# Kernel tuning notes

Hardware: AMD Instinct MI355X
Metric: run time of the kernel (lower is better)

## Reference

```python
import jax, jax.numpy as jnp
import numpy as np

B, T = 65536, 200
H, S, P = 512, 1000, 5
EPS = 1e-6


def setup_inputs() -> dict:
    key = jax.random.key(0)
    ks = jax.random.split(key, 8)
    init = lambda k, shp, fan: (jax.random.normal(k, shp, jnp.float32) / np.float32(np.sqrt(fan)))
    return {
        "X": jax.random.randint(ks[0], (B,), 0, S, dtype=jnp.int32),
        "y": jax.random.randint(ks[1], (B, T), 0, 2, dtype=jnp.int32),
        "embed": init(ks[2], (S, H), 1.0),
        "W1": init(ks[3], (H, H), H), "b1": jnp.zeros((H,), jnp.float32),
        "W2": init(ks[4], (H, H), H), "b2": jnp.zeros((H,), jnp.float32),
        "Wout": init(ks[5], (H, P), H), "bout": jnp.zeros((P,), jnp.float32),
    }


def reference(X, y, embed, W1, b1, W2, b2, Wout, bout):
    # --- MLP over skill embeddings: params (B, 5) = (l, f, g, s, latent0) ---
    e = embed[X]                                    # (B, H)
    h = jax.nn.relu(e @ W1 + b1)                    # num_layers = 2
    h = jax.nn.relu(h @ W2 + b2)
    params = jnp.clip(jax.nn.sigmoid(h @ Wout + bout), EPS, 1.0 - EPS)  # (B, 5)
    l, g, s = params[:, 0], params[:, 2], params[:, 3]
    latent0 = params[:, 4]                          # (B,)

    y_clean = jnp.where(y == -1, 0, y).astype(jnp.float32)  # (B, T)

    # --- BKT latent-update recurrence over T steps ---
    def step(latent, y_t):
        num1 = latent * (1.0 - s)
        correct = num1 + (1.0 - latent) * g
        k_t1 = num1 / correct
        k_t0 = latent * s / (latent * s + (1.0 - latent) * (1.0 - g))
        k_t = jnp.where(y_t > 0.5, k_t1, k_t0)
        nxt = jnp.clip(k_t + (1.0 - k_t) * l, EPS, 1.0 - EPS)
        return nxt, (correct, latent)

    _, (corrects, latents) = jax.lax.scan(step, latent0, y_clean.T)  # (T, B) each
    return corrects.T, latents.T, params
```

## Files before the change

### kernel.cpp

```cpp
#include <hip/hip_runtime.h>


typedef unsigned int uint;
typedef unsigned short ushort_t;
typedef __attribute__((ext_vector_type(8))) short short8;
typedef __attribute__((ext_vector_type(4))) float f32x4;

#define SS 1000
#define HH 512
#define TT 200
#define BB_ 65536
#define PP 5

#define OFF_EMB   0
#define OFF_B1    512000
#define OFF_B2    512512
#define OFF_WOUT  513024
#define OFF_BOUT  515584
#define CONV_TOT  515589

__device__ __forceinline__ float b2f(ushort_t u) {
    return __uint_as_float(((uint)u) << 16);
}
__device__ __forceinline__ ushort_t f2b(float f) {
    uint u = __float_as_uint(f);
    uint r = u + 0x7FFFu + ((u >> 16) & 1u);
    return (ushort_t)(r >> 16);
}
__device__ __forceinline__ int detect_bf16(const uint* __restrict__ embed_raw,
                                           int tid) {
    uint w = embed_raw[tid & 63];
    uint e = (w >> 7) & 0xFFu;
    bool pl = (e >= 117u && e <= 130u);
    return __popcll(__ballot(pl)) >= 32 ? 1 : 0;
}
__device__ __forceinline__ ushort_t ld_bf16(const void* src, int idx, int fb) {
    return fb ? ((const ushort_t*)src)[idx] : f2b(((const float*)src)[idx]);
}

__device__ __forceinline__ float bkt_step(float latent, bool yt,
                                          float oms, float omg, float A1,
                                          float A0, float g, float s,
                                          float oml, float l,
                                          float* correct_out) {
    float num1    = latent * oms;
    float correct = fmaf(latent, A1, g);
    float lats    = latent * s;
    float num = yt ? num1 : lats;
    float den = yt ? correct : fmaf(latent, A0, omg);
    float kt  = num * __builtin_amdgcn_rcpf(den);
    *correct_out = correct;
    float nxt = fmaf(kt, oml, l);
    return fminf(fmaxf(nxt, 1e-6f), 1.f - 1e-6f);
}

__global__ __launch_bounds__(256) void prep_kernel(
    const void* __restrict__ embed, const void* __restrict__ W1,
    const void* __restrict__ b1,    const void* __restrict__ W2,
    const void* __restrict__ b2,    const void* __restrict__ Wout,
    const void* __restrict__ bout,
    ushort_t* __restrict__ conv, ushort_t* __restrict__ WT1,
    ushort_t* __restrict__ WT2)
{
    int tid = threadIdx.x;
    int fb = detect_bf16((const uint*)embed, tid);
    int bx = blockIdx.x;
    if (bx < 2015) {
        int i = bx * 256 + tid;
        if (i < CONV_TOT) {
            const void* src; int off;
            if      (i < OFF_B1)   { src = embed; off = i; }
            else if (i < OFF_B2)   { src = b1;    off = i - OFF_B1; }
            else if (i < OFF_WOUT) { src = b2;    off = i - OFF_B2; }
            else if (i < OFF_BOUT) { src = Wout;  off = i - OFF_WOUT; }
            else                   { src = bout;  off = i - OFF_BOUT; }
            conv[i] = ld_bf16(src, off, fb);
        }
    } else {
        __shared__ ushort_t t[32][33];
        int bi = bx - 2015;
        const void* W = bi < 256 ? W1 : W2;
        ushort_t* WT = bi < 256 ? WT1 : WT2;
        int ti = bi & 255;
        int k0 = (ti & 15) * 32, n0 = (ti >> 4) * 32;
        int tx = tid & 31, ty = tid >> 5;
        #pragma unroll
        for (int i = ty; i < 32; i += 8)
            t[i][tx] = ld_bf16(W, (k0 + i) * HH + n0 + tx, fb);
        __syncthreads();
        #pragma unroll
        for (int i = ty; i < 32; i += 8)
            WT[(n0 + i) * HH + k0 + tx] = t[tx][i];
    }
}

__global__ __launch_bounds__(256) void mlp_layer(
    const ushort_t* __restrict__ A, const ushort_t* __restrict__ WT,
    const ushort_t* __restrict__ bias, ushort_t* __restrict__ H, int Mclamp)
{
    int tid = threadIdx.x;
    int lane = tid & 63;
    int wave = tid >> 6;
    int m_base = blockIdx.x * 64 + wave * 16;
    int n_base = blockIdx.y * 16;
    int lrow = lane & 15;
    int q = lane >> 4;
    int rowA = m_base + lrow; if (rowA > Mclamp) rowA = Mclamp;

    const short8* Ap = (const short8*)(A + (size_t)rowA * HH) + q;
    const short8* Bp = (const short8*)(WT + (size_t)(n_base + lrow) * HH) + q;

    f32x4 acc = {0.f, 0.f, 0.f, 0.f};
    #pragma unroll 8
    for (int kk = 0; kk < 16; kk++) {
        short8 a = Ap[kk * 4];
        short8 b = Bp[kk * 4];
        acc = __builtin_amdgcn_mfma_f32_16x16x32_bf16(a, b, acc, 0, 0, 0);
    }

    int orow = m_base + q * 4;
    int n = n_base + lrow;
    float bb = b2f(bias[n]);
    #pragma unroll
    for (int r = 0; r < 4; r++) {
        float v = acc[r] + bb;
        H[(size_t)(orow + r) * HH + n] = f2b(fmaxf(v, 0.f));
    }
}

__global__ __launch_bounds__(256) void params_kernel(
    const ushort_t* __restrict__ h2, const ushort_t* __restrict__ conv,
    float* __restrict__ table)
{
    int wid = blockIdx.x * 4 + (threadIdx.x >> 6);
    int lane = threadIdx.x & 63;
    if (wid >= SS * PP) return;
    int row = wid / PP, p = wid - row * PP;
    const ushort_t* Wout = conv + OFF_WOUT;
    const ushort_t* bout = conv + OFF_BOUT;
    const short8* hr = (const short8*)(h2 + (size_t)row * HH);
    short8 h = hr[lane];
    float acc = 0.f;
    #pragma unroll
    for (int j = 0; j < 8; j++) {
        int k = lane * 8 + j;
        acc += b2f((ushort_t)h[j]) * b2f(Wout[k * PP + p]);
    }
    #pragma unroll
    for (int m = 32; m; m >>= 1) acc += __shfl_xor(acc, m);
    if (lane == 0) {
        float x = acc + b2f(bout[p]);
        float sg = 1.f / (1.f + expf(-x));
        sg = fminf(fmaxf(sg, 1e-6f), 1.f - 1e-6f);
        table[(size_t)row * 8 + p] = sg;
    }
}

__global__ __launch_bounds__(256) void scan_a(
    const int* __restrict__ X, const int* __restrict__ y,
    const float* __restrict__ table,
    float* __restrict__ cpA, uint* __restrict__ maskA)
{
    int r = blockIdx.x * 256 + threadIdx.x;
    const int4* yrow = (const int4*)(y + (size_t)r * TT);
    uint u[8] = {0, 0, 0, 0, 0, 0, 0, 0};
    #pragma unroll
    for (int k = 0; k < 50; k++) {
        int4 v = yrow[k];
        int t = 4 * k;
        u[(t + 0) / 25] |= (uint)(v.x == 1) << ((t + 0) % 25);
        u[(t + 1) / 25] |= (uint)(v.y == 1) << ((t + 1) % 25);
        u[(t + 2) / 25] |= (uint)(v.z == 1) << ((t + 2) % 25);
        u[(t + 3) / 25] |= (uint)(v.w == 1) << ((t + 3) % 25);
    }

    int xi = X[r]; xi = xi < 0 ? 0 : (xi >= SS ? SS - 1 : xi);
    float l      = table[xi * 8 + 0];
    float g      = table[xi * 8 + 2];
    float s      = table[xi * 8 + 3];
    float latent = table[xi * 8 + 4];
    float oms = 1.f - s, omg = 1.f - g, oml = 1.f - l;
    float A1 = 1.f - s - g, A0 = s + g - 1.f;

    float cp[8];
    #pragma unroll
    for (int w = 0; w < 8; w++) {
        cp[w] = latent;
        uint uw = u[w];
        #pragma unroll
        for (int i = 0; i < 25; i++) {
            float cdummy;
            latent = bkt_step(latent, (uw >> i) & 1u,
                              oms, omg, A1, A0, g, s, oml, l, &cdummy);
        }
    }
    #pragma unroll
    for (int w = 0; w < 8; w++) {
        cpA[(size_t)w * BB_ + r]   = cp[w];
        maskA[(size_t)w * BB_ + r] = u[w];
    }
}

__global__ __launch_bounds__(256) void scan_b(
    const int* __restrict__ X, const float* __restrict__ table,
    const float* __restrict__ cpA, const uint* __restrict__ maskA,
    const uint* __restrict__ embed_raw, void* __restrict__ out)
{
    __shared__ __align__(16) float stg[32 * 200];
    int tid = blockIdx.x * 256 + threadIdx.x;
    int r = tid >> 3;
    int j = tid & 7;
    int lr = threadIdx.x >> 3;
    int rbase = blockIdx.x * 32;
    int fb = detect_bf16(embed_raw, threadIdx.x);

    int xi = X[r]; xi = xi < 0 ? 0 : (xi >= SS ? SS - 1 : xi);
    float l  = table[xi * 8 + 0];
    float p1 = table[xi * 8 + 1];
    float g  = table[xi * 8 + 2];
    float s  = table[xi * 8 + 3];
    float L0 = table[xi * 8 + 4];

    if (j < 5) {
        float pv = j == 0 ? l : j == 1 ? p1 : j == 2 ? g : j == 3 ? s : L0;
        size_t po = 2ull * BB_ * TT + (size_t)r * 5 + j;
        if (fb) ((ushort_t*)out)[po] = f2b(pv);
        else    ((float*)out)[po] = pv;
    }

    float latent = cpA[(size_t)j * BB_ + r];
    uint  u      = maskA[(size_t)j * BB_ + r];
    float oms = 1.f - s, omg = 1.f - g, oml = 1.f - l;
    float A1 = 1.f - s - g, A0 = s + g - 1.f;

    if (fb) {
        ushort_t* cgb = (ushort_t*)out;
        ushort_t* lgb = (ushort_t*)out + (size_t)BB_ * TT;
        size_t eoff = (size_t)r * TT + j * 25;
        #pragma unroll
        for (int i = 0; i < 25; i++) {
            float correct;
            float nxt = bkt_step(latent, (u >> i) & 1u,
                                 oms, omg, A1, A0, g, s, oml, l, &correct);
            cgb[eoff + i] = f2b(correct);
            lgb[eoff + i] = f2b(latent);
            latent = nxt;
        }
        return;
    }

    float lat_arr[25];
    int sbase = lr * 200 + j * 25;
    #pragma unroll
    for (int i = 0; i < 25; i++) {
        float correct;
        float nxt = bkt_step(latent, (u >> i) & 1u,
                             oms, omg, A1, A0, g, s, oml, l, &correct);
        stg[sbase + i] = correct;
        lat_arr[i] = latent;
        latent = nxt;
    }
    __syncthreads();
    {
        const uint4* src = (const uint4*)stg;
        uint4* dst = (uint4*)((float*)out + (size_t)rbase * TT);
        for (int idx = threadIdx.x; idx < 1600; idx += 256)
            dst[idx] = src[idx];
    }
    __syncthreads();
    #pragma unroll
    for (int i = 0; i < 25; i++)
        stg[sbase + i] = lat_arr[i];
    __syncthreads();
    {
        const uint4* src = (const uint4*)stg;
        uint4* dst = (uint4*)((float*)out + (size_t)BB_ * TT + (size_t)rbase * TT);
        for (int idx = threadIdx.x; idx < 1600; idx += 256)
            dst[idx] = src[idx];
    }
}

extern "C" void kernel_launch(void* const* d_in, const int* in_sizes, int n_in,
                              void* d_out, int out_size, void* d_ws, size_t ws_size,
                              hipStream_t stream) {
    const int* X = (const int*)d_in[0];
    const int* y = (const int*)d_in[1];

    char* ws = (char*)d_ws;
    ushort_t* conv  = (ushort_t*)(ws);
    ushort_t* WT1   = (ushort_t*)(ws + 1048576);
    ushort_t* WT2   = (ushort_t*)(ws + 1572864);
    ushort_t* h1    = (ushort_t*)(ws + 2097152);
    ushort_t* h2    = (ushort_t*)(ws + 3145728);
    float*    table = (float*)(ws + 4194304);
    float*    cpA   = (float*)(ws + 4227072);
    uint*     maskA = (uint*)(ws + 6324224);

    prep_kernel<<<dim3(2527, 1, 1), 256, 0, stream>>>(
        d_in[2], d_in[3], d_in[4], d_in[5], d_in[6], d_in[7], d_in[8],
        conv, WT1, WT2);
    mlp_layer<<<dim3(16, 32, 1), 256, 0, stream>>>(conv + OFF_EMB, WT1, conv + OFF_B1, h1, SS - 1);
    mlp_layer<<<dim3(16, 32, 1), 256, 0, stream>>>(h1, WT2, conv + OFF_B2, h2, 1023);
    params_kernel<<<dim3(1250, 1, 1), 256, 0, stream>>>(h2, conv, table);
    scan_a<<<dim3(BB_ / 256, 1, 1), 256, 0, stream>>>(X, y, table, cpA, maskA);
    scan_b<<<dim3((BB_ * 8) / 256, 1, 1), 256, 0, stream>>>(
        X, table, cpA, maskA, (const uint*)d_in[2], (void*)d_out);
}
```

Measured before the change: 208.9 us.

## Fuse MLP prep stages into cooperative kernel and merge scan passes

Prep, both MLP layers and the params projection now run in one cooperative kernel separated by grid syncs, replacing four launches. The two scan kernels become one: each block packs its y rows into shared-memory bits, one thread per row computes the segment checkpoints into shared memory, and 8 threads per row then produce the outputs. This drops the global cpA/maskA round trip and the launch gaps between stages. Output copies use nontemporal stores. The risk is that the checkpoint pass runs serially on 32 threads per block while the other threads wait, which limits parallelism inside each block.

```diff
diff --git a/kernel.cpp b/kernel.cpp
--- a/kernel.cpp
+++ b/kernel.cpp
@@ -1,10 +1,14 @@
 #include <hip/hip_runtime.h>
+#include <hip/hip_cooperative_groups.h>
+namespace cg = cooperative_groups;
 
 
 typedef unsigned int uint;
+typedef unsigned char uchar;
 typedef unsigned short ushort_t;
 typedef __attribute__((ext_vector_type(8))) short short8;
 typedef __attribute__((ext_vector_type(4))) float f32x4;
+typedef __attribute__((ext_vector_type(4))) uint uint4v;
 
 #define SS 1000
 #define HH 512
@@ -54,55 +58,13 @@
     return fminf(fmaxf(nxt, 1e-6f), 1.f - 1e-6f);
 }
 
-__global__ __launch_bounds__(256) void prep_kernel(
-    const void* __restrict__ embed, const void* __restrict__ W1,
-    const void* __restrict__ b1,    const void* __restrict__ W2,
-    const void* __restrict__ b2,    const void* __restrict__ Wout,
-    const void* __restrict__ bout,
-    ushort_t* __restrict__ conv, ushort_t* __restrict__ WT1,
-    ushort_t* __restrict__ WT2)
+__device__ __forceinline__ void mlp_tile(
+    const ushort_t* __restrict__ A, const ushort_t* __restrict__ WT,
+    const ushort_t* __restrict__ bias, ushort_t* __restrict__ H,
+    int Mclamp, int id, int lane)
 {
-    int tid = threadIdx.x;
-    int fb = detect_bf16((const uint*)embed, tid);
-    int bx = blockIdx.x;
-    if (bx < 2015) {
-        int i = bx * 256 + tid;
-        if (i < CONV_TOT) {
-            const void* src; int off;
-            if      (i < OFF_B1)   { src = embed; off = i; }
-            else if (i < OFF_B2)   { src = b1;    off = i - OFF_B1; }
-            else if (i < OFF_WOUT) { src = b2;    off = i - OFF_B2; }
-            else if (i < OFF_BOUT) { src = Wout;  off = i - OFF_WOUT; }
-            else                   { src = bout;  off = i - OFF_BOUT; }
-            conv[i] = ld_bf16(src, off, fb);
-        }
-    } else {
-        __shared__ ushort_t t[32][33];
-        int bi = bx - 2015;
-        const void* W = bi < 256 ? W1 : W2;
-        ushort_t* WT = bi < 256 ? WT1 : WT2;
-        int ti = bi & 255;
-        int k0 = (ti & 15) * 32, n0 = (ti >> 4) * 32;
-        int tx = tid & 31, ty = tid >> 5;
-        #pragma unroll
-        for (int i = ty; i < 32; i += 8)
-            t[i][tx] = ld_bf16(W, (k0 + i) * HH + n0 + tx, fb);
-        __syncthreads();
-        #pragma unroll
-        for (int i = ty; i < 32; i += 8)
-            WT[(n0 + i) * HH + k0 + tx] = t[tx][i];
-    }
-}
-
-__global__ __launch_bounds__(256) void mlp_layer(
-    const ushort_t* __restrict__ A, const ushort_t* __restrict__ WT,
-    const ushort_t* __restrict__ bias, ushort_t* __restrict__ H, int Mclamp)
-{
-    int tid = threadIdx.x;
-    int lane = tid & 63;
-    int wave = tid >> 6;
-    int m_base = blockIdx.x * 64 + wave * 16;
-    int n_base = blockIdx.y * 16;
+    int m_base = (id & 63) * 16;
+    int n_base = (id >> 6) * 16;
     int lrow = lane & 15;
     int q = lane >> 4;
     int rowA = m_base + lrow; if (rowA > Mclamp) rowA = Mclamp;
@@ -117,7 +79,6 @@
         short8 b = Bp[kk * 4];
         acc = __builtin_amdgcn_mfma_f32_16x16x32_bf16(a, b, acc, 0, 0, 0);
     }
-
     int orow = m_base + q * 4;
     int n = n_base + lrow;
     float bb = b2f(bias[n]);
@@ -128,93 +89,126 @@
     }
 }
 
-__global__ __launch_bounds__(256) void params_kernel(
-    const ushort_t* __restrict__ h2, const ushort_t* __restrict__ conv,
-    float* __restrict__ table)
+__global__ __launch_bounds__(256, 2) void aux_kernel(
+    const void* embed, const void* W1, const void* b1, const void* W2,
+    const void* b2, const void* Wout, const void* bout,
+    ushort_t* conv, ushort_t* WT1, ushort_t* WT2,
+    ushort_t* h1, ushort_t* h2, float* table)
 {
-    int wid = blockIdx.x * 4 + (threadIdx.x >> 6);
-    int lane = threadIdx.x & 63;
-    if (wid >= SS * PP) return;
-    int row = wid / PP, p = wid - row * PP;
-    const ushort_t* Wout = conv + OFF_WOUT;
-    const ushort_t* bout = conv + OFF_BOUT;
-    const short8* hr = (const short8*)(h2 + (size_t)row * HH);
-    short8 h = hr[lane];
-    float acc = 0.f;
-    #pragma unroll
-    for (int j = 0; j < 8; j++) {
-        int k = lane * 8 + j;
-        acc += b2f((ushort_t)h[j]) * b2f(Wout[k * PP + p]);
-    }
-    #pragma unroll
-    for (int m = 32; m; m >>= 1) acc += __shfl_xor(acc, m);
-    if (lane == 0) {
-        float x = acc + b2f(bout[p]);
-        float sg = 1.f / (1.f + expf(-x));
-        sg = fminf(fmaxf(sg, 1e-6f), 1.f - 1e-6f);
-        table[(size_t)row * 8 + p] = sg;
-    }
-}
-
-__global__ __launch_bounds__(256) void scan_a(
+    cg::grid_group grid = cg::this_grid();
+    __shared__ ushort_t t[32][33];
+    int tid = threadIdx.x;
+    int bx = blockIdx.x;
+    int lane = tid & 63;
+    int wave = tid >> 6;
+    int fb = detect_bf16((const uint*)embed, tid);
+
+    for (int i = bx * 256 + tid; i < CONV_TOT; i += 512 * 256) {
+        const void* src; int off;
+        if      (i < OFF_B1)   { src = embed; off = i; }
+        else if (i < OFF_B2)   { src = b1;    off = i - OFF_B1; }
+        else if (i < OFF_WOUT) { src = b2;    off = i - OFF_B2; }
+        else if (i < OFF_BOUT) { src = Wout;  off = i - OFF_WOUT; }
+        else                   { src = bout;  off = i - OFF_BOUT; }
+        conv[i] = ld_bf16(src, off, fb);
+    }
+    {
+        const void* W = bx < 256 ? W1 : W2;
+        ushort_t* WT = bx < 256 ? WT1 : WT2;
+        int ti = bx & 255;
+        int k0 = (ti & 15) * 32, n0 = (ti >> 4) * 32;
+        int tx = tid & 31, ty = tid >> 5;
+        #pragma unroll
+        for (int i = ty; i < 32; i += 8)
+            t[i][tx] = ld_bf16(W, (k0 + i) * HH + n0 + tx, fb);
+        __syncthreads();
+        #pragma unroll
+        for (int i = ty; i < 32; i += 8)
+            WT[(n0 + i) * HH + k0 + tx] = t[tx][i];
+    }
+    grid.sync();
+
+    int id = bx * 4 + wave;
+    mlp_tile(conv + OFF_EMB, WT1, conv + OFF_B1, h1, SS - 1, id, lane);
+    grid.sync();
+    mlp_tile(h1, WT2, conv + OFF_B2, h2, 1023, id, lane);
+    grid.sync();
+
+    const ushort_t* WoutC = conv + OFF_WOUT;
+    const ushort_t* boutC = conv + OFF_BOUT;
+    for (int wid = id; wid < SS * PP; wid += 2048) {
+        int row = wid / PP, p = wid - row * PP;
+        const short8* hr = (const short8*)(h2 + (size_t)row * HH);
+        short8 h = hr[lane];
+        float acc = 0.f;
+        #pragma unroll
+        for (int j = 0; j < 8; j++) {
+            int k = lane * 8 + j;
+            acc += b2f((ushort_t)h[j]) * b2f(WoutC[k * PP + p]);
+        }
+        #pragma unroll
+        for (int m = 32; m; m >>= 1) acc += __shfl_xor(acc, m);
+        if (lane == 0) {
+            float x = acc + b2f(boutC[p]);
+            float sg = 1.f / (1.f + expf(-x));
+            sg = fminf(fmaxf(sg, 1e-6f), 1.f - 1e-6f);
+            table[(size_t)row * 8 + p] = sg;
+        }
+    }
+}
+
+__global__ __launch_bounds__(256) void scan_kernel(
     const int* __restrict__ X, const int* __restrict__ y,
-    const float* __restrict__ table,
-    float* __restrict__ cpA, uint* __restrict__ maskA)
-{
-    int r = blockIdx.x * 256 + threadIdx.x;
-    const int4* yrow = (const int4*)(y + (size_t)r * TT);
-    uint u[8] = {0, 0, 0, 0, 0, 0, 0, 0};
-    #pragma unroll
-    for (int k = 0; k < 50; k++) {
-        int4 v = yrow[k];
-        int t = 4 * k;
-        u[(t + 0) / 25] |= (uint)(v.x == 1) << ((t + 0) % 25);
-        u[(t + 1) / 25] |= (uint)(v.y == 1) << ((t + 1) % 25);
-        u[(t + 2) / 25] |= (uint)(v.z == 1) << ((t + 2) % 25);
-        u[(t + 3) / 25] |= (uint)(v.w == 1) << ((t + 3) % 25);
-    }
-
-    int xi = X[r]; xi = xi < 0 ? 0 : (xi >= SS ? SS - 1 : xi);
-    float l      = table[xi * 8 + 0];
-    float g      = table[xi * 8 + 2];
-    float s      = table[xi * 8 + 3];
-    float latent = table[xi * 8 + 4];
-    float oms = 1.f - s, omg = 1.f - g, oml = 1.f - l;
-    float A1 = 1.f - s - g, A0 = s + g - 1.f;
-
-    float cp[8];
-    #pragma unroll
-    for (int w = 0; w < 8; w++) {
-        cp[w] = latent;
-        uint uw = u[w];
-        #pragma unroll
-        for (int i = 0; i < 25; i++) {
-            float cdummy;
-            latent = bkt_step(latent, (uw >> i) & 1u,
-                              oms, omg, A1, A0, g, s, oml, l, &cdummy);
-        }
-    }
-    #pragma unroll
-    for (int w = 0; w < 8; w++) {
-        cpA[(size_t)w * BB_ + r]   = cp[w];
-        maskA[(size_t)w * BB_ + r] = u[w];
-    }
-}
-
-__global__ __launch_bounds__(256) void scan_b(
-    const int* __restrict__ X, const float* __restrict__ table,
-    const float* __restrict__ cpA, const uint* __restrict__ maskA,
-    const uint* __restrict__ embed_raw, void* __restrict__ out)
+    const float* __restrict__ table, const uint* __restrict__ embed_raw,
+    void* __restrict__ out)
 {
     __shared__ __align__(16) float stg[32 * 200];
-    int tid = blockIdx.x * 256 + threadIdx.x;
-    int r = tid >> 3;
-    int j = tid & 7;
-    int lr = threadIdx.x >> 3;
+    __shared__ uchar ybit[32 * 50];
+    __shared__ float cpL[8 * 32];
+    __shared__ uint  maskL[8 * 32];
+    int tid = threadIdx.x;
     int rbase = blockIdx.x * 32;
-    int fb = detect_bf16(embed_raw, threadIdx.x);
-
-    int xi = X[r]; xi = xi < 0 ? 0 : (xi >= SS ? SS - 1 : xi);
+    int fb = detect_bf16(embed_raw, tid);
+
+    for (int idx = tid; idx < 1600; idx += 256) {
+        int r = idx / 50, k = idx - r * 50;
+        int4 v = *(const int4*)(y + (size_t)(rbase + r) * TT + k * 4);
+        uint nib = (uint)(v.x == 1) | ((uint)(v.y == 1) << 1) |
+                   ((uint)(v.z == 1) << 2) | ((uint)(v.w == 1) << 3);
+        ybit[r * 50 + k] = (uchar)nib;
+    }
+    __syncthreads();
+
+    if (tid < 32) {
+        int rg = rbase + tid;
+        int xi = X[rg]; xi = xi < 0 ? 0 : (xi >= SS ? SS - 1 : xi);
+        float l      = table[xi * 8 + 0];
+        float g      = table[xi * 8 + 2];
+        float s      = table[xi * 8 + 3];
+        float latent = table[xi * 8 + 4];
+        float oms = 1.f - s, omg = 1.f - g, oml = 1.f - l;
+        float A1 = 1.f - s - g, A0 = s + g - 1.f;
+        int base = tid * 50;
+        #pragma unroll
+        for (int w = 0; w < 8; w++) {
+            cpL[w * 32 + tid] = latent;
+            uint m = 0;
+            #pragma unroll
+            for (int i = 0; i < 25; i++) {
+                int t_ = w * 25 + i;
+                uint bit = (ybit[base + (t_ >> 2)] >> (t_ & 3)) & 1u;
+                m |= bit << i;
+                float cd;
+                latent = bkt_step(latent, bit, oms, omg, A1, A0, g, s, oml, l, &cd);
+            }
+            maskL[w * 32 + tid] = m;
+        }
+    }
+    __syncthreads();
+
+    int r = tid >> 3, j = tid & 7;
+    int rg = rbase + r;
+    int xi = X[rg]; xi = xi < 0 ? 0 : (xi >= SS ? SS - 1 : xi);
     float l  = table[xi * 8 + 0];
     float p1 = table[xi * 8 + 1];
     float g  = table[xi * 8 + 2];
@@ -223,20 +217,20 @@
 
     if (j < 5) {
         float pv = j == 0 ? l : j == 1 ? p1 : j == 2 ? g : j == 3 ? s : L0;
-        size_t po = 2ull * BB_ * TT + (size_t)r * 5 + j;
+        size_t po = 2ull * BB_ * TT + (size_t)rg * 5 + j;
         if (fb) ((ushort_t*)out)[po] = f2b(pv);
         else    ((float*)out)[po] = pv;
     }
 
-    float latent = cpA[(size_t)j * BB_ + r];
-    uint  u      = maskA[(size_t)j * BB_ + r];
+    float latent = cpL[j * 32 + r];
+    uint  u      = maskL[j * 32 + r];
     float oms = 1.f - s, omg = 1.f - g, oml = 1.f - l;
     float A1 = 1.f - s - g, A0 = s + g - 1.f;
 
     if (fb) {
         ushort_t* cgb = (ushort_t*)out;
         ushort_t* lgb = (ushort_t*)out + (size_t)BB_ * TT;
-        size_t eoff = (size_t)r * TT + j * 25;
+        size_t eoff = (size_t)rg * TT + j * 25;
         #pragma unroll
         for (int i = 0; i < 25; i++) {
             float correct;
@@ -250,7 +244,7 @@
     }
 
     float lat_arr[25];
-    int sbase = lr * 200 + j * 25;
+    int sbase = r * 200 + j * 25;
     #pragma unroll
     for (int i = 0; i < 25; i++) {
         float correct;
@@ -262,10 +256,10 @@
     }
     __syncthreads();
     {
-        const uint4* src = (const uint4*)stg;
-        uint4* dst = (uint4*)((float*)out + (size_t)rbase * TT);
-        for (int idx = threadIdx.x; idx < 1600; idx += 256)
-            dst[idx] = src[idx];
+        const uint4v* src = (const uint4v*)stg;
+        uint4v* dst = (uint4v*)((float*)out + (size_t)rbase * TT);
+        for (int idx = tid; idx < 1600; idx += 256)
+            __builtin_nontemporal_store(src[idx], dst + idx);
     }
     __syncthreads();
     #pragma unroll
@@ -273,10 +267,10 @@
         stg[sbase + i] = lat_arr[i];
     __syncthreads();
     {
-        const uint4* src = (const uint4*)stg;
-        uint4* dst = (uint4*)((float*)out + (size_t)BB_ * TT + (size_t)rbase * TT);
-        for (int idx = threadIdx.x; idx < 1600; idx += 256)
-            dst[idx] = src[idx];
+        const uint4v* src = (const uint4v*)stg;
+        uint4v* dst = (uint4v*)((float*)out + (size_t)BB_ * TT + (size_t)rbase * TT);
+        for (int idx = tid; idx < 1600; idx += 256)
+            __builtin_nontemporal_store(src[idx], dst + idx);
     }
 }
 
@@ -293,16 +287,19 @@
     ushort_t* h1    = (ushort_t*)(ws + 2097152);
     ushort_t* h2    = (ushort_t*)(ws + 3145728);
     float*    table = (float*)(ws + 4194304);
-    float*    cpA   = (float*)(ws + 4227072);
-    uint*     maskA = (uint*)(ws + 6324224);
-
-    prep_kernel<<<dim3(2527, 1, 1), 256, 0, stream>>>(
-        d_in[2], d_in[3], d_in[4], d_in[5], d_in[6], d_in[7], d_in[8],
-        conv, WT1, WT2);
-    mlp_layer<<<dim3(16, 32, 1), 256, 0, stream>>>(conv + OFF_EMB, WT1, conv + OFF_B1, h1, SS - 1);
-    mlp_layer<<<dim3(16, 32, 1), 256, 0, stream>>>(h1, WT2, conv + OFF_B2, h2, 1023);
-    params_kernel<<<dim3(1250, 1, 1), 256, 0, stream>>>(h2, conv, table);
-    scan_a<<<dim3(BB_ / 256, 1, 1), 256, 0, stream>>>(X, y, table, cpA, maskA);
-    scan_b<<<dim3((BB_ * 8) / 256, 1, 1), 256, 0, stream>>>(
-        X, table, cpA, maskA, (const uint*)d_in[2], (void*)d_out);
-}
+
+    const void* embed = d_in[2];
+    const void* W1v   = d_in[3];
+    const void* b1v   = d_in[4];
+    const void* W2v   = d_in[5];
+    const void* b2v   = d_in[6];
+    const void* Woutv = d_in[7];
+    const void* boutv = d_in[8];
+
+    void* args[] = { &embed, &W1v, &b1v, &W2v, &b2v, &Woutv, &boutv,
+                     &conv, &WT1, &WT2, &h1, &h2, &table };
+    hipLaunchCooperativeKernel((const void*)aux_kernel, dim3(512), dim3(256),
+                               args, 0u, stream);
+    scan_kernel<<<dim3(2048, 1, 1), 256, 0, stream>>>(
+        X, y, table, (const uint*)d_in[2], (void*)d_out);
+}
```

Result: slower. 399.3 us (+91.1%).
